# Optimization experiments

Hardware: AMD Instinct MI355X
Metric: run time of the kernel (lower is better)

## Reference

```python
import jax, jax.numpy as jnp
import numpy as np
import math

DEC = (4, 4, 4)  # (vertical=Y, horizontal=X, depth=Z)


def _idct_mat(N, dtype=jnp.float32):
    # orthonormal DCT-II matrix D[k,n]; IDCT (DCT-III ortho) is D.T
    k = jnp.arange(N, dtype=dtype)[:, None]
    n = jnp.arange(N, dtype=dtype)[None, :]
    D = jnp.cos(jnp.pi * (n + 0.5) * k / N)
    s = jnp.where(k == 0, jnp.sqrt(1.0 / N), jnp.sqrt(2.0 / N))
    return (s * D).T  # [n, k]: y[n] = sum_k IDCT[n,k] X[k]


def _permute_idct_coefs(x, dec):
    decY, decX, decZ = dec
    coefs = x.reshape(-1, decY * decX * decZ)
    chY, chX, chZ = (decY + 1) // 2, (decX + 1) // 2, (decZ + 1) // 2
    fhY, fhX, fhZ = decY // 2, decX // 2, decZ // 2
    sizes = [(chY, chX, chZ), (chY, chX, fhZ), (chY, fhX, chZ), (chY, fhX, fhZ),
             (fhY, chX, chZ), (fhY, chX, fhZ), (fhY, fhX, chZ), (fhY, fhX, fhZ)]
    nB = coefs.shape[0]
    value = jnp.zeros((nB, decY, decX, decZ), dtype=x.dtype)
    slices = [(slice(0, None, 2), slice(0, None, 2), slice(0, None, 2)),
              (slice(0, None, 2), slice(0, None, 2), slice(1, None, 2)),
              (slice(0, None, 2), slice(1, None, 2), slice(0, None, 2)),
              (slice(0, None, 2), slice(1, None, 2), slice(1, None, 2)),
              (slice(1, None, 2), slice(0, None, 2), slice(0, None, 2)),
              (slice(1, None, 2), slice(0, None, 2), slice(1, None, 2)),
              (slice(1, None, 2), slice(1, None, 2), slice(0, None, 2)),
              (slice(1, None, 2), slice(1, None, 2), slice(1, None, 2))]
    start = 0
    for (sy, sx, sz), (ny, nx, nz) in zip(slices, sizes):
        n = ny * nx * nz
        chunk = coefs[:, start:start + n].reshape(nB, ny, nx, nz)
        value = value.at[:, sy, sx, sz].set(chunk)
        start += n
    return value


def setup_inputs() -> dict:
    key = jax.random.key(0)
    x0 = jax.random.normal(key, (4, 64, 64, 64, DEC[0] * DEC[1] * DEC[2]), dtype=jnp.float32)
    return {"x0": x0}


def reference(x0) -> jnp.ndarray:
    nsamples, nrows, ncols, nlays, _ = x0.shape
    decY, decX, decZ = DEC
    V = _permute_idct_coefs(x0, DEC)  # [nBlocks, decY, decX, decZ]
    IY, IX, IZ = _idct_mat(decY, x0.dtype), _idct_mat(decX, x0.dtype), _idct_mat(decZ, x0.dtype)
    # separable 3D IDCT (orthonormal) along the three block axes
    Y = jnp.einsum('byxz,iy,jx,kz->bijk', V, IY, IX, IZ)
    height, width, depth = nrows * decY, ncols * decX, nlays * decZ
    Z = Y.reshape(nsamples, 1, height, width, depth)
    return Z
```

## Files before the change

### kernel.cpp

```cpp
#include <hip/hip_runtime.h>


#define WG 64
#define ROWS 68

#define C1F 0.6532814824381883f
#define C3F 0.2705980500730985f

#define IDCT4(a0, a2, a1, a3, r0, r1, r2, r3)            \
    {                                                    \
        const float e0 = 0.5f * ((a0) + (a2));           \
        const float e1 = 0.5f * ((a0) - (a2));           \
        const float o0 = C1F * (a1) + C3F * (a3);        \
        const float o1 = C3F * (a1) - C1F * (a3);        \
        (r0) = e0 + o0;                                  \
        (r1) = e1 + o1;                                  \
        (r2) = e1 - o1;                                  \
        (r3) = e0 - o0;                                  \
    }

__global__ __launch_bounds__(WG) void nsolt_idct3d_kernel(
    const float* __restrict__ in, float* __restrict__ out)
{
    __shared__ float lds[WG * ROWS];
    const int t = threadIdx.x;
    const size_t base = (size_t)blockIdx.x * (WG * 64);

#pragma unroll
    for (int m = 0; m < 16; ++m) {
        const int e = m * (WG * 4) + t * 4;
        const float4 q = *reinterpret_cast<const float4*>(in + base + e);
        const int row = e >> 6;
        const int col = e & 63;
        *reinterpret_cast<float4*>(&lds[row * ROWS + col]) = q;
    }
    __syncthreads();

    float* __restrict__ myrow = &lds[t * ROWS];

    float A[4][4][4];
#pragma unroll
    for (int c2 = 0; c2 < 2; ++c2) {
#pragma unroll
        for (int w2 = 0; w2 < 2; ++w2) {
            const int y = 2 * w2 + c2;
#pragma unroll
            for (int c1 = 0; c1 < 2; ++c1) {
                const int b0 = c2 * 32 + c1 * 16 + w2 * 4;
                const float4 q0 = *reinterpret_cast<const float4*>(&myrow[b0]);
                const float4 q1 = *reinterpret_cast<const float4*>(&myrow[b0 + 8]);
                IDCT4(q0.x, q0.y, q1.x, q1.y,
                      A[y][c1][0], A[y][c1][1], A[y][c1][2], A[y][c1][3]);
                IDCT4(q0.z, q0.w, q1.z, q1.w,
                      A[y][2 + c1][0], A[y][2 + c1][1], A[y][2 + c1][2], A[y][2 + c1][3]);
            }
        }
    }

    float B[4][4][4];
#pragma unroll
    for (int y = 0; y < 4; ++y) {
#pragma unroll
        for (int n = 0; n < 4; ++n) {
            IDCT4(A[y][0][n], A[y][2][n], A[y][1][n], A[y][3][n],
                  B[y][0][n], B[y][1][n], B[y][2][n], B[y][3][n]);
        }
    }

#pragma unroll
    for (int j = 0; j < 4; ++j) {
#pragma unroll
        for (int n = 0; n < 4; ++n) {
            float r0, r1, r2, r3;
            IDCT4(B[0][j][n], B[2][j][n], B[1][j][n], B[3][j][n], r0, r1, r2, r3);
            myrow[0 * 16 + j * 4 + n] = r0;
            myrow[1 * 16 + j * 4 + n] = r1;
            myrow[2 * 16 + j * 4 + n] = r2;
            myrow[3 * 16 + j * 4 + n] = r3;
        }
    }
    __syncthreads();

#pragma unroll
    for (int m = 0; m < 16; ++m) {
        const int e = m * (WG * 4) + t * 4;
        const int row = e >> 6;
        const int col = e & 63;
        const float4 q = *reinterpret_cast<const float4*>(&lds[row * ROWS + col]);
        *reinterpret_cast<float4*>(out + base + e) = q;
    }
}

extern "C" void kernel_launch(void* const* d_in, const int* in_sizes, int n_in,
                              void* d_out, int out_size, void* d_ws, size_t ws_size,
                              hipStream_t stream)
{
    const float* in = (const float*)d_in[0];
    float* out = (float*)d_out;

    const long long nBlocks = (long long)in_sizes[0] / 64;
    const int grid = (int)(nBlocks / WG);

    hipLaunchKernelGGL(nsolt_idct3d_kernel, dim3(grid), dim3(WG), 0, stream,
                       in, out);
}
```

Before: 100.1 us.

## Split each block across four lanes with shuffles and direct global-to-LDS loads

Each 64-coefficient block is now handled by four lanes instead of one thread. The X and Y butterfly stages exchange partial sums through lane shuffles, and the workgroup grows from 64 to 256 threads. Input is loaded straight into LDS with global_load_lds using an XOR-swizzled layout, replacing the padded-row staging through registers. The aim is to cut per-thread register pressure and LDS bank conflicts and to raise occupancy for this memory-bound kernel, at the cost of extra shuffles and more intricate swizzle indexing.

Result: no change. 99.96 us (-0.1%).

```diff
diff --git a/kernel.cpp b/kernel.cpp
--- a/kernel.cpp
+++ b/kernel.cpp
@@ -1,9 +1,7 @@
 #include <hip/hip_runtime.h>
 
 
-#define WG 64
-#define ROWS 68
-
+#define WG 256
 #define C1F 0.6532814824381883f
 #define C3F 0.2705980500730985f
 
@@ -22,72 +20,118 @@
 __global__ __launch_bounds__(WG) void nsolt_idct3d_kernel(
     const float* __restrict__ in, float* __restrict__ out)
 {
-    __shared__ float lds[WG * ROWS];
+    __shared__ float lds[64 * 64];
     const int t = threadIdx.x;
-    const size_t base = (size_t)blockIdx.x * (WG * 64);
+    const int w = t >> 6;
+    const int l = t & 63;
+    const size_t wgbase = (size_t)blockIdx.x * 4096;
 
+    {
+        const int c   = l & 15;
+        const int rlo = l >> 4;
 #pragma unroll
-    for (int m = 0; m < 16; ++m) {
-        const int e = m * (WG * 4) + t * 4;
-        const float4 q = *reinterpret_cast<const float4*>(in + base + e);
-        const int row = e >> 6;
-        const int col = e & 63;
-        *reinterpret_cast<float4*>(&lds[row * ROWS + col]) = q;
-    }
-    __syncthreads();
-
-    float* __restrict__ myrow = &lds[t * ROWS];
-
-    float A[4][4][4];
-#pragma unroll
-    for (int c2 = 0; c2 < 2; ++c2) {
-#pragma unroll
-        for (int w2 = 0; w2 < 2; ++w2) {
-            const int y = 2 * w2 + c2;
-#pragma unroll
-            for (int c1 = 0; c1 < 2; ++c1) {
-                const int b0 = c2 * 32 + c1 * 16 + w2 * 4;
-                const float4 q0 = *reinterpret_cast<const float4*>(&myrow[b0]);
-                const float4 q1 = *reinterpret_cast<const float4*>(&myrow[b0 + 8]);
-                IDCT4(q0.x, q0.y, q1.x, q1.y,
-                      A[y][c1][0], A[y][c1][1], A[y][c1][2], A[y][c1][3]);
-                IDCT4(q0.z, q0.w, q1.z, q1.w,
-                      A[y][2 + c1][0], A[y][2 + c1][1], A[y][2 + c1][2], A[y][2 + c1][3]);
-            }
-        }
-    }
-
-    float B[4][4][4];
-#pragma unroll
-    for (int y = 0; y < 4; ++y) {
-#pragma unroll
-        for (int n = 0; n < 4; ++n) {
-            IDCT4(A[y][0][n], A[y][2][n], A[y][1][n], A[y][3][n],
-                  B[y][0][n], B[y][1][n], B[y][2][n], B[y][3][n]);
-        }
-    }
-
-#pragma unroll
-    for (int j = 0; j < 4; ++j) {
-#pragma unroll
-        for (int n = 0; n < 4; ++n) {
-            float r0, r1, r2, r3;
-            IDCT4(B[0][j][n], B[2][j][n], B[1][j][n], B[3][j][n], r0, r1, r2, r3);
-            myrow[0 * 16 + j * 4 + n] = r0;
-            myrow[1 * 16 + j * 4 + n] = r1;
-            myrow[2 * 16 + j * 4 + n] = r2;
-            myrow[3 * 16 + j * 4 + n] = r3;
+        for (int m = 0; m < 4; ++m) {
+            const int r = w * 16 + m * 4 + rlo;
+            const int h = (r << 4) | (c ^ rlo ^ (4 * (m & 1)));
+            const float* src = in + wgbase + (size_t)h * 4;
+            __builtin_amdgcn_global_load_lds(
+                (const __attribute__((address_space(1))) void*)src,
+                (__attribute__((address_space(3))) void*)(&lds[(w * 256 + m * 64) * 4]),
+                16, 0, 0);
         }
     }
     __syncthreads();
 
+    const int gW = t >> 2;
+    const int j  = t & 3;
+    const int c1 = j & 1;
+    const int c2 = j >> 1;
+    const int s7 = gW & 7;
+    float* __restrict__ myblk = &lds[gW * 64];
+
+    float qa[16];
 #pragma unroll
-    for (int m = 0; m < 16; ++m) {
-        const int e = m * (WG * 4) + t * 4;
-        const int row = e >> 6;
-        const int col = e & 63;
-        const float4 q = *reinterpret_cast<const float4*>(&lds[row * ROWS + col]);
-        *reinterpret_cast<float4*>(out + base + e) = q;
+    for (int k = 0; k < 4; ++k) {
+        const float4 v = *reinterpret_cast<const float4*>(
+            &myblk[(((4 * j + k) ^ s7) << 2)]);
+        qa[k * 4 + 0] = v.x; qa[k * 4 + 1] = v.y;
+        qa[k * 4 + 2] = v.z; qa[k * 4 + 3] = v.w;
+    }
+
+    float A[2][2][4];
+#pragma unroll
+    for (int w2 = 0; w2 < 2; ++w2) {
+#pragma unroll
+        for (int w1 = 0; w1 < 2; ++w1) {
+            const float a0 = qa[w2 * 4 + 2 * w1];
+            const float a2 = qa[w2 * 4 + 2 * w1 + 1];
+            const float a1 = qa[(2 + w2) * 4 + 2 * w1];
+            const float a3 = qa[(2 + w2) * 4 + 2 * w1 + 1];
+            IDCT4(a0, a2, a1, a3,
+                  A[w2][w1][0], A[w2][w1][1], A[w2][w1][2], A[w2][w1][3]);
+        }
+    }
+
+    const float xk0 = c1 ? C3F : 0.5f;
+    const float xk1 = c1 ? -C1F : 0.5f;
+    const float xs0 = c1 ? C1F : 0.5f;
+    const float xs1 = c1 ? C3F : -0.5f;
+    const float xsg = c1 ? -1.0f : 1.0f;
+
+    float X[2][2][4];
+#pragma unroll
+    for (int w2 = 0; w2 < 2; ++w2) {
+#pragma unroll
+        for (int n = 0; n < 4; ++n) {
+            const float A0 = A[w2][0][n], A1 = A[w2][1][n];
+            const float uk = xk0 * A0 + xk1 * A1;
+            const float us = xs0 * A0 + xs1 * A1;
+            const float rv = __shfl_xor(us, 1, 64);
+            X[w2][0][n] = uk + rv;
+            X[w2][1][n] = xsg * (uk - rv);
+        }
+    }
+
+    const float yk0 = c2 ? C3F : 0.5f;
+    const float yk1 = c2 ? -C1F : 0.5f;
+    const float ys0 = c2 ? C1F : 0.5f;
+    const float ys1 = c2 ? C3F : -0.5f;
+    const float ysg = c2 ? -1.0f : 1.0f;
+
+    const int xa = c1 ? 1 : 0, xb = c1 ? 2 : 3;
+    const int ya = c2 ? 1 : 0, yb = c2 ? 2 : 3;
+
+#pragma unroll
+    for (int xs = 0; xs < 2; ++xs) {
+        float ra[4], rb[4];
+#pragma unroll
+        for (int n = 0; n < 4; ++n) {
+            const float A0 = X[0][xs][n], A1 = X[1][xs][n];
+            const float uk = yk0 * A0 + yk1 * A1;
+            const float us = ys0 * A0 + ys1 * A1;
+            const float rv = __shfl_xor(us, 2, 64);
+            ra[n] = uk + rv;
+            rb[n] = ysg * (uk - rv);
+        }
+        const int xv = xs ? xb : xa;
+        float4 va; va.x = ra[0]; va.y = ra[1]; va.z = ra[2]; va.w = ra[3];
+        float4 vb; vb.x = rb[0]; vb.y = rb[1]; vb.z = rb[2]; vb.w = rb[3];
+        *reinterpret_cast<float4*>(&myblk[(((ya * 4 + xv) ^ s7) << 2)]) = va;
+        *reinterpret_cast<float4*>(&myblk[(((yb * 4 + xv) ^ s7) << 2)]) = vb;
+    }
+    __syncthreads();
+
+    {
+        const int c   = l & 15;
+        const int rlo = l >> 4;
+#pragma unroll
+        for (int m = 0; m < 4; ++m) {
+            const int f = w * 256 + m * 64 + l;
+            const float4 v = *reinterpret_cast<const float4*>(&lds[f * 4]);
+            const int r = w * 16 + m * 4 + rlo;
+            const int h = (r << 4) | (c ^ rlo ^ (4 * (m & 1)));
+            *reinterpret_cast<float4*>(out + wgbase + (size_t)h * 4) = v;
+        }
     }
 }
 
@@ -99,7 +143,7 @@
     float* out = (float*)d_out;
 
     const long long nBlocks = (long long)in_sizes[0] / 64;
-    const int grid = (int)(nBlocks / WG);
+    const int grid = (int)(nBlocks / 64);
 
     hipLaunchKernelGGL(nsolt_idct3d_kernel, dim3(grid), dim3(WG), 0, stream,
                        in, out);
```
